# Optimization experiments

Hardware: AMD Instinct MI355X
Metric: run time of the kernel (lower is better)

## Reference

```python
import jax, jax.numpy as jnp
import numpy as np

N = 100000
E = 3200000
D = 64


def setup_inputs() -> dict:
    key = jax.random.key(0)
    k1, k2, k3 = jax.random.split(key, 3)
    indices = jax.random.randint(k1, (2, E), 0, N, dtype=jnp.int64) if jax.config.jax_enable_x64 else jax.random.randint(k1, (2, E), 0, N, dtype=jnp.int32)
    values = jax.random.uniform(k2, (E,), dtype=jnp.float32)
    b = jax.random.normal(k3, (N, D), dtype=jnp.float32)
    return {"indices": indices, "values": values, "shape": N, "b": b}


def reference(indices, values, shape, b):
    # sparse COO [N,N] @ dense [N,D]:
    # out[r] = sum over edges e with row[e]==r of values[e] * b[col[e]]
    row, col = indices[0], indices[1]
    msgs = values[:, None] * b[col]            # [E, D] gather + scale
    out = jax.ops.segment_sum(msgs, row, num_segments=shape)  # [N, D] scatter-add
    return out
```

## Files before the change

### kernel.cpp

```cpp
#include <hip/hip_runtime.h>
#include <hip/hip_bf16.h>


#define D 64
#define BROWS 64
#define MAXNB 2048
#define CAP 2560
#define NM (CAP / 256)
#define SPILLCAP 8192
#define NCHUNK 4
#define NBINS (BROWS * NCHUNK)

#define CROWS 2048
#define NCB 64
#define NREP 8
#define SCH_A 4096
#define CBLK 4352
#define NBLK_C 16
#define CAPC8 (CBLK * 2)
#define NCONV 1024

__global__ __launch_bounds__(256) void spmm_atomic_kernel(
    const int* __restrict__ rows, const int* __restrict__ cols,
    const float* __restrict__ vals, const float* __restrict__ b,
    float* __restrict__ out, int E) {
  long long gid = (long long)blockIdx.x * blockDim.x + threadIdx.x;
  int e = (int)(gid >> 6);
  int d = (int)(gid & 63);
  if (e >= E) return;
  atomicAdd(&out[(long long)rows[e] * D + d], vals[e] * b[(long long)cols[e] * D + d]);
}

__device__ __forceinline__ unsigned bf16rne(float x) {
  unsigned u = __float_as_uint(x);
  return (u + 0x7FFFu + ((u >> 16) & 1u)) >> 16;
}
__global__ __launch_bounds__(256) void coarse_conv_kernel(
    const int* __restrict__ rows, const int* __restrict__ cols,
    const float* __restrict__ vals, int* __restrict__ gcoarse,
    uint2* __restrict__ cslab_lo, uint2* __restrict__ cslab_hi, int csplitV,
    uint4* __restrict__ spill, int* __restrict__ spill_cnt, int E, int nco,
    const float4* __restrict__ bsrc, uint2* __restrict__ b16, int n4) {
  __shared__ uint2 stage[SCH_A];
  __shared__ unsigned char sbin[SCH_A];
  __shared__ int h[NCB];
  __shared__ int lst[NCB];
  __shared__ int gb[NCB];
  int t = threadIdx.x;

  if (blockIdx.x >= nco) {
    for (int i = (blockIdx.x - nco) * 256 + t; i < n4; i += NCONV * 256) {
      float4 f = bsrc[i];
      b16[i] = make_uint2(bf16rne(f.x) | (bf16rne(f.y) << 16),
                          bf16rne(f.z) | (bf16rne(f.w) << 16));
    }
    return;
  }

  int rep = blockIdx.x & (NREP - 1);
  if (t < NCB) h[t] = 0;
  __syncthreads();
  int start = blockIdx.x * SCH_A;
  int ec = E - start;
  if (ec > SCH_A) ec = SCH_A;
  bool full = (start + SCH_A <= E);

  int4 r4[4];
  int rank[16];
  if (full) {
#pragma unroll
    for (int ki = 0; ki < 4; ki++) {
      r4[ki] = ((const int4*)(rows + start + ki * 1024))[t];
      rank[4 * ki + 0] = atomicAdd(&h[r4[ki].x >> 11], 1);
      rank[4 * ki + 1] = atomicAdd(&h[r4[ki].y >> 11], 1);
      rank[4 * ki + 2] = atomicAdd(&h[r4[ki].z >> 11], 1);
      rank[4 * ki + 3] = atomicAdd(&h[r4[ki].w >> 11], 1);
    }
  } else {
#pragma unroll
    for (int ki = 0; ki < 4; ki++) {
      int e = start + ki * 1024 + t * 4;
      int4 rr = make_int4(-1, -1, -1, -1);
      if (e + 0 < E) { rr.x = rows[e + 0]; rank[4 * ki + 0] = atomicAdd(&h[rr.x >> 11], 1); }
      if (e + 1 < E) { rr.y = rows[e + 1]; rank[4 * ki + 1] = atomicAdd(&h[rr.y >> 11], 1); }
      if (e + 2 < E) { rr.z = rows[e + 2]; rank[4 * ki + 2] = atomicAdd(&h[rr.z >> 11], 1); }
      if (e + 3 < E) { rr.w = rows[e + 3]; rank[4 * ki + 3] = atomicAdd(&h[rr.w >> 11], 1); }
      r4[ki] = rr;
    }
  }
  __syncthreads();
  if (t < NCB) {
    int c = h[t];
    int x = c;
#pragma unroll
    for (int off = 1; off < 64; off <<= 1) {
      int u = __shfl_up(x, off);
      if (t >= off) x += u;
    }
    lst[t] = x - c;
    gb[t] = c ? atomicAdd(&gcoarse[t * NREP + rep], c) : 0;
  }
  __syncthreads();
#pragma unroll
  for (int ki = 0; ki < 4; ki++) {
    int e = start + ki * 1024 + t * 4;
    int rr[4] = {r4[ki].x, r4[ki].y, r4[ki].z, r4[ki].w};
    int cc[4];
    float vv[4];
    if (full) {
      int4 c4 = ((const int4*)(cols + start + ki * 1024))[t];
      float4 v4 = ((const float4*)(vals + start + ki * 1024))[t];
      cc[0] = c4.x; cc[1] = c4.y; cc[2] = c4.z; cc[3] = c4.w;
      vv[0] = v4.x; vv[1] = v4.y; vv[2] = v4.z; vv[3] = v4.w;
    } else {
#pragma unroll
      for (int j = 0; j < 4; j++) {
        cc[j] = (e + j < E) ? cols[e + j] : 0;
        vv[j] = (e + j < E) ? vals[e + j] : 0.f;
      }
    }
#pragma unroll
    for (int j = 0; j < 4; j++) {
      if (e + j < E) {
        int r = rr[j];
        int bn = r >> 11;
        int pos = lst[bn] + rank[4 * ki + j];
        stage[pos] = make_uint2(((unsigned)(r & (CROWS - 1)) << 17) |
                                    (unsigned)cc[j],
                                __float_as_uint(vv[j]));
        sbin[pos] = (unsigned char)bn;
      }
    }
  }
  __syncthreads();
  for (int i = t; i < ec; i += 256) {
    int bn = sbin[i];
    uint2 p = stage[i];
    int pin = gb[bn] + (i - lst[bn]);
    if (pin < CAPC8) {
      int v = bn * NREP + rep;
      uint2* slab = (v < csplitV) ? (cslab_lo + (size_t)v * CAPC8)
                                  : (cslab_hi + (size_t)(v - csplitV) * CAPC8);
      slab[pin] = p;
    } else {
      int sp = atomicAdd(spill_cnt, 1);
      if (sp < SPILLCAP)
        spill[sp] = make_uint4((unsigned)((bn << 11) | (int)(p.x >> 17)),
                               p.x & 0x1FFFFu, p.y, 0u);
    }
  }
}

__global__ __launch_bounds__(256) void fine_scatter_kernel(
    const int* __restrict__ gcoarse, const uint2* __restrict__ cslab_lo,
    const uint2* __restrict__ cslab_hi, int csplitV, int* __restrict__ gcount,
    uint2* __restrict__ pairs, uint4* __restrict__ spill,
    int* __restrict__ spill_cnt) {
  int c = blockIdx.x >> 4;
  int sub = blockIdx.x & 15;
  int v = c * NREP + (sub >> 1);
  int cnt = gcoarse[v];
  if (cnt > CAPC8) cnt = CAPC8;
  int base = (sub & 1) * CBLK;
  int ec = cnt - base;
  if (ec <= 0) return;
  if (ec > CBLK) ec = CBLK;
  const uint2* src = ((v < csplitV) ? (cslab_lo + (size_t)v * CAPC8)
                                    : (cslab_hi + (size_t)(v - csplitV) * CAPC8)) +
                     base;
  __shared__ uint2 stage[CBLK];
  __shared__ unsigned char sbin[CBLK];
  __shared__ int h[32];
  __shared__ int lst[32];
  __shared__ int gb[32];
  int t = threadIdx.x;
  if (t < 32) h[t] = 0;
  __syncthreads();
  uint2 mine[17];
  int rank[17];
#pragma unroll
  for (int k = 0; k < 17; k++) {
    int i = k * 256 + t;
    if (i < ec) {
      mine[k] = src[i];
      rank[k] = atomicAdd(&h[mine[k].x >> 23], 1);
    }
  }
  __syncthreads();
  if (t < 32) {
    int cn = h[t];
    int x = cn;
#pragma unroll
    for (int off = 1; off < 32; off <<= 1) {
      int u = __shfl_up(x, off);
      if (t >= off) x += u;
    }
    lst[t] = x - cn;
    gb[t] = cn ? atomicAdd(&gcount[c * 32 + t], cn) : 0;
  }
  __syncthreads();
#pragma unroll
  for (int k = 0; k < 17; k++) {
    int i = k * 256 + t;
    if (i < ec) {
      uint2 p = mine[k];
      int f = (int)(p.x >> 23);
      int pos = lst[f] + rank[k];
      unsigned key2 = (((p.x >> 17) & 63u) << 26) | ((p.x & 0x1FFFFu) << 7);
      stage[pos] = make_uint2(key2, p.y);
      sbin[pos] = (unsigned char)f;
    }
  }
  __syncthreads();
  for (int i = t; i < ec; i += 256) {
    int f = sbin[i];
    uint2 p = stage[i];
    int pin = gb[f] + (i - lst[f]);
    int gbkt = c * 32 + f;
    if (pin < CAP) {
      pairs[(size_t)gbkt * CAP + pin] = p;
    } else {
      int sp = atomicAdd(spill_cnt, 1);
      if (sp < SPILLCAP)
        spill[sp] = make_uint4((unsigned)(gbkt * BROWS + (int)(p.x >> 26)),
                               (p.x >> 7) & 0x1FFFFu, p.y, 0u);
    }
  }
}

__global__ __launch_bounds__(256) void spmm_fused_kernel(
    const uint2* __restrict__ pairs, const int* __restrict__ gcount,
    const uint2* __restrict__ b16, float* __restrict__ out, int N,
    const uint4* __restrict__ spill, const int* __restrict__ spill_cnt) {
  __shared__ uint2 lp[CAP];
  __shared__ int cnt[NBINS];
  __shared__ int roff[NBINS + 1];
  __shared__ int wpart[4];
  int bkt = blockIdx.x;
  int cntE = gcount[bkt];
  if (cntE > CAP) cntE = CAP;
  const uint2* src = pairs + (size_t)bkt * CAP;
  int t = threadIdx.x;
  int lane = t & 63;
  int wv = t >> 6;
  if (t < NBINS) cnt[t] = 0;
  __syncthreads();
  uint2 mine[NM];
  int rk[NM];
#pragma unroll
  for (int k = 0; k < NM; k++) {
    int i = t + k * 256;
    if (i < cntE) {
      mine[k] = src[i];
      int bin = ((mine[k].x >> 26) << 2) | ((mine[k].x >> 22) & 3);
      rk[k] = atomicAdd(&cnt[bin], 1);
    }
  }
  __syncthreads();
  {
    int c0 = cnt[t];
    int x = c0;
#pragma unroll
    for (int off = 1; off < 64; off <<= 1) {
      int u = __shfl_up(x, off);
      if (lane >= off) x += u;
    }
    if (lane == 63) wpart[wv] = x;
    __syncthreads();
    int wbase = 0;
    for (int w = 0; w < wv; w++) wbase += wpart[w];
    roff[t] = wbase + x - c0;
    if (t == 255) roff[NBINS] = wbase + x;
  }
  __syncthreads();
#pragma unroll
  for (int k = 0; k < NM; k++) {
    int i = t + k * 256;
    if (i < cntE) {
      int bin = ((mine[k].x >> 26) << 2) | ((mine[k].x >> 22) & 3);
      lp[roff[bin] + rk[k]] = make_uint2(mine[k].x & 0x03FFFF80u, mine[k].y);
    }
  }
  __syncthreads();
  int g = lane >> 3;
  int l8 = lane & 7;
  int gid32 = wv * 8 + g;
  const char* bq = (const char*)b16 + (l8 << 4);
  int row_base = bkt * BROWS;
  float acc[2][8] = {{0.f, 0.f, 0.f, 0.f, 0.f, 0.f, 0.f, 0.f},
                     {0.f, 0.f, 0.f, 0.f, 0.f, 0.f, 0.f, 0.f}};
  for (int ch = 0; ch < NCHUNK; ch++) {
#pragma unroll
    for (int rr = 0; rr < 2; rr++) {
      int r = gid32 + 32 * rr;
      int bin = (r << 2) | ch;
      int j0 = roff[bin], j1 = roff[bin + 1];
      for (int base = j0; base < j1; base += 4) {
        uint4 bv[4];
        float vv[4];
#pragma unroll
        for (int k = 0; k < 4; k++) {
          int idx = base + k;
          int ic = (idx < j1) ? idx : j0;
          uint2 p = lp[ic];
          bv[k] = *(const uint4*)(bq + p.x);
          vv[k] = (idx < j1) ? __uint_as_float(p.y) : 0.f;
        }
#pragma unroll
        for (int k = 0; k < 4; k++) {
          unsigned u0 = bv[k].x, u1 = bv[k].y, u2 = bv[k].z, u3 = bv[k].w;
          float v = vv[k];
          acc[rr][0] += v * __uint_as_float(u0 << 16);
          acc[rr][1] += v * __uint_as_float(u0 & 0xFFFF0000u);
          acc[rr][2] += v * __uint_as_float(u1 << 16);
          acc[rr][3] += v * __uint_as_float(u1 & 0xFFFF0000u);
          acc[rr][4] += v * __uint_as_float(u2 << 16);
          acc[rr][5] += v * __uint_as_float(u2 & 0xFFFF0000u);
          acc[rr][6] += v * __uint_as_float(u3 << 16);
          acc[rr][7] += v * __uint_as_float(u3 & 0xFFFF0000u);
        }
      }
    }
  }
  int nsp = *spill_cnt;
  if (nsp > 0) {
    if (nsp > SPILLCAP) nsp = SPILLCAP;
    for (int s = 0; s < nsp; s++) {
      uint4 e = spill[s];
      int rg = (int)e.x;
      if ((rg >> 6) != bkt) continue;
      int rl = rg & 63;
#pragma unroll
      for (int rr = 0; rr < 2; rr++) {
        if (rl == gid32 + 32 * rr) {
          uint4 bv = *(const uint4*)((const char*)b16 +
                                     ((size_t)e.y << 7) + (l8 << 4));
          float v = __uint_as_float(e.z);
          acc[rr][0] += v * __uint_as_float(bv.x << 16);
          acc[rr][1] += v * __uint_as_float(bv.x & 0xFFFF0000u);
          acc[rr][2] += v * __uint_as_float(bv.y << 16);
          acc[rr][3] += v * __uint_as_float(bv.y & 0xFFFF0000u);
          acc[rr][4] += v * __uint_as_float(bv.z << 16);
          acc[rr][5] += v * __uint_as_float(bv.z & 0xFFFF0000u);
          acc[rr][6] += v * __uint_as_float(bv.w << 16);
          acc[rr][7] += v * __uint_as_float(bv.w & 0xFFFF0000u);
        }
      }
    }
  }
#pragma unroll
  for (int rr = 0; rr < 2; rr++) {
    int gr = row_base + gid32 + 32 * rr;
    if (gr < N) {
      float4* dst = (float4*)(out + (size_t)gr * D + l8 * 8);
      dst[0] = make_float4(acc[rr][0], acc[rr][1], acc[rr][2], acc[rr][3]);
      dst[1] = make_float4(acc[rr][4], acc[rr][5], acc[rr][6], acc[rr][7]);
    }
  }
}

extern "C" void kernel_launch(void* const* d_in, const int* in_sizes, int n_in,
                              void* d_out, int out_size, void* d_ws, size_t ws_size,
                              hipStream_t stream) {
  const int* indices = (const int*)d_in[0];
  const float* vals  = (const float*)d_in[1];
  const float* b     = (const float*)d_in[3];

  int E = in_sizes[1];
  int N = in_sizes[3] / D;
  const int* rows = indices;
  const int* cols = indices + E;

  int NC = (N + CROWS - 1) / CROWS;
  int NCV = NC * NREP;
  int n4 = N * D / 4;

  size_t off_gcount  = 0;
  size_t off_gcoarse = off_gcount + (size_t)MAXNB * 4;
  size_t off_scnt    = off_gcoarse + (size_t)NCB * NREP * 4;
  size_t off_spill   = (off_scnt + 4 + 15) & ~(size_t)15;
  size_t off_pairs   = off_spill + (size_t)SPILLCAP * 16;
  size_t npbkt       = (size_t)NC * 32;
  size_t off_b16     = off_pairs + npbkt * CAP * 8;
  size_t off_cextra  = off_b16 + (size_t)N * D * 2;
  size_t outbytes    = (size_t)out_size * 4;
  int csplitV = (int)(outbytes / ((size_t)CAPC8 * 8));
  if (csplitV > NCV) csplitV = NCV;
  size_t cextra = (size_t)(NCV - csplitV) * CAPC8 * 8;
  size_t need2 = off_cextra + cextra;

  if (ws_size >= need2 && NC <= NCB && (int)npbkt <= MAXNB) {
    char*  ws        = (char*)d_ws;
    int*   gcount    = (int*)(ws + off_gcount);
    int*   gcoarse   = (int*)(ws + off_gcoarse);
    int*   spill_cnt = (int*)(ws + off_scnt);
    uint4* spill     = (uint4*)(ws + off_spill);
    uint2* pairs     = (uint2*)(ws + off_pairs);
    uint2* b16       = (uint2*)(ws + off_b16);
    uint2* cslab_lo  = (uint2*)d_out;
    uint2* cslab_hi  = (uint2*)(ws + off_cextra);

    hipMemsetAsync(gcount, 0,
                   (size_t)MAXNB * 4 + (size_t)NCB * NREP * 4 + 4, stream);
    int nco = (E + SCH_A - 1) / SCH_A;
    coarse_conv_kernel<<<nco + NCONV, 256, 0, stream>>>(
        rows, cols, vals, gcoarse, cslab_lo, cslab_hi, csplitV,
        spill, spill_cnt, E, nco, (const float4*)b, b16, n4);
    fine_scatter_kernel<<<NC * NBLK_C, 256, 0, stream>>>(
        gcoarse, cslab_lo, cslab_hi, csplitV, gcount, pairs, spill, spill_cnt);
    spmm_fused_kernel<<<(int)npbkt, 256, 0, stream>>>(
        pairs, gcount, b16, (float*)d_out, N, spill, spill_cnt);
    return;
  }

  hipMemsetAsync(d_out, 0, (size_t)out_size * sizeof(float), stream);
  long long total = (long long)E * 64;
  spmm_atomic_kernel<<<(int)((total + 255) / 256), 256, 0, stream>>>(
      rows, cols, vals, b, (float*)d_out, E);
}
```

Baseline: 212.3 us.

## Drop fine scatter pass; fused kernel filters coarse slabs directly per bucket

Removes the fine_scatter kernel and its pairs buffer. Each fused SpMM block now scans all 8 replica slabs of its coarse row group twice, once to count and once to place, keeping only entries for its 64-row bucket. A shared-memory overflow list and a block-index swizzle for L2 locality are added. This removes one kernel launch and a global write/read of all edges, but each block now reads 32x more slab data than it keeps (filtering), which relies on L2 reuse across sibling buckets.

```diff
diff --git a/kernel.cpp b/kernel.cpp
--- a/kernel.cpp
+++ b/kernel.cpp
@@ -4,20 +4,17 @@
 
 #define D 64
 #define BROWS 64
-#define MAXNB 2048
 #define CAP 2560
-#define NM (CAP / 256)
 #define SPILLCAP 8192
 #define NCHUNK 4
 #define NBINS (BROWS * NCHUNK)
+#define OVFCAP 64
 
 #define CROWS 2048
 #define NCB 64
 #define NREP 8
 #define SCH_A 4096
-#define CBLK 4352
-#define NBLK_C 16
-#define CAPC8 (CBLK * 2)
+#define CAPC8 8704
 #define NCONV 1024
 
 __global__ __launch_bounds__(256) void spmm_atomic_kernel(
@@ -38,7 +35,7 @@
 __global__ __launch_bounds__(256) void coarse_conv_kernel(
     const int* __restrict__ rows, const int* __restrict__ cols,
     const float* __restrict__ vals, int* __restrict__ gcoarse,
-    uint2* __restrict__ cslab_lo, uint2* __restrict__ cslab_hi, int csplitV,
+    uint2* __restrict__ cslab,
     uint4* __restrict__ spill, int* __restrict__ spill_cnt, int E, int nco,
     const float4* __restrict__ bsrc, uint2* __restrict__ b16, int n4) {
   __shared__ uint2 stage[SCH_A];
@@ -138,10 +135,7 @@
     uint2 p = stage[i];
     int pin = gb[bn] + (i - lst[bn]);
     if (pin < CAPC8) {
-      int v = bn * NREP + rep;
-      uint2* slab = (v < csplitV) ? (cslab_lo + (size_t)v * CAPC8)
-                                  : (cslab_hi + (size_t)(v - csplitV) * CAPC8);
-      slab[pin] = p;
+      cslab[(size_t)(bn * NREP + rep) * CAPC8 + pin] = p;
     } else {
       int sp = atomicAdd(spill_cnt, 1);
       if (sp < SPILLCAP)
@@ -151,109 +145,36 @@
   }
 }
 
-__global__ __launch_bounds__(256) void fine_scatter_kernel(
-    const int* __restrict__ gcoarse, const uint2* __restrict__ cslab_lo,
-    const uint2* __restrict__ cslab_hi, int csplitV, int* __restrict__ gcount,
-    uint2* __restrict__ pairs, uint4* __restrict__ spill,
-    int* __restrict__ spill_cnt) {
-  int c = blockIdx.x >> 4;
-  int sub = blockIdx.x & 15;
-  int v = c * NREP + (sub >> 1);
-  int cnt = gcoarse[v];
-  if (cnt > CAPC8) cnt = CAPC8;
-  int base = (sub & 1) * CBLK;
-  int ec = cnt - base;
-  if (ec <= 0) return;
-  if (ec > CBLK) ec = CBLK;
-  const uint2* src = ((v < csplitV) ? (cslab_lo + (size_t)v * CAPC8)
-                                    : (cslab_hi + (size_t)(v - csplitV) * CAPC8)) +
-                     base;
-  __shared__ uint2 stage[CBLK];
-  __shared__ unsigned char sbin[CBLK];
-  __shared__ int h[32];
-  __shared__ int lst[32];
-  __shared__ int gb[32];
-  int t = threadIdx.x;
-  if (t < 32) h[t] = 0;
-  __syncthreads();
-  uint2 mine[17];
-  int rank[17];
-#pragma unroll
-  for (int k = 0; k < 17; k++) {
-    int i = k * 256 + t;
-    if (i < ec) {
-      mine[k] = src[i];
-      rank[k] = atomicAdd(&h[mine[k].x >> 23], 1);
-    }
-  }
-  __syncthreads();
-  if (t < 32) {
-    int cn = h[t];
-    int x = cn;
-#pragma unroll
-    for (int off = 1; off < 32; off <<= 1) {
-      int u = __shfl_up(x, off);
-      if (t >= off) x += u;
-    }
-    lst[t] = x - cn;
-    gb[t] = cn ? atomicAdd(&gcount[c * 32 + t], cn) : 0;
-  }
-  __syncthreads();
-#pragma unroll
-  for (int k = 0; k < 17; k++) {
-    int i = k * 256 + t;
-    if (i < ec) {
-      uint2 p = mine[k];
-      int f = (int)(p.x >> 23);
-      int pos = lst[f] + rank[k];
-      unsigned key2 = (((p.x >> 17) & 63u) << 26) | ((p.x & 0x1FFFFu) << 7);
-      stage[pos] = make_uint2(key2, p.y);
-      sbin[pos] = (unsigned char)f;
-    }
-  }
-  __syncthreads();
-  for (int i = t; i < ec; i += 256) {
-    int f = sbin[i];
-    uint2 p = stage[i];
-    int pin = gb[f] + (i - lst[f]);
-    int gbkt = c * 32 + f;
-    if (pin < CAP) {
-      pairs[(size_t)gbkt * CAP + pin] = p;
-    } else {
-      int sp = atomicAdd(spill_cnt, 1);
-      if (sp < SPILLCAP)
-        spill[sp] = make_uint4((unsigned)(gbkt * BROWS + (int)(p.x >> 26)),
-                               (p.x >> 7) & 0x1FFFFu, p.y, 0u);
-    }
-  }
-}
-
 __global__ __launch_bounds__(256) void spmm_fused_kernel(
-    const uint2* __restrict__ pairs, const int* __restrict__ gcount,
-    const uint2* __restrict__ b16, float* __restrict__ out, int N,
+    const int* __restrict__ gcoarse, const uint2* __restrict__ cslab,
+    const uint2* __restrict__ b16, float* __restrict__ out, int N, int swz,
     const uint4* __restrict__ spill, const int* __restrict__ spill_cnt) {
   __shared__ uint2 lp[CAP];
   __shared__ int cnt[NBINS];
   __shared__ int roff[NBINS + 1];
+  __shared__ int wcur[NBINS];
   __shared__ int wpart[4];
-  int bkt = blockIdx.x;
-  int cntE = gcount[bkt];
-  if (cntE > CAP) cntE = CAP;
-  const uint2* src = pairs + (size_t)bkt * CAP;
+  __shared__ uint2 ovf[OVFCAP];
+  __shared__ int ovfn;
+  int bid = blockIdx.x;
+  int bkt = swz ? ((bid & 7) * swz + (bid >> 3)) : bid;
+  int c = bkt >> 5;
+  unsigned f = (unsigned)(bkt & 31);
   int t = threadIdx.x;
   int lane = t & 63;
   int wv = t >> 6;
   if (t < NBINS) cnt[t] = 0;
-  __syncthreads();
-  uint2 mine[NM];
-  int rk[NM];
-#pragma unroll
-  for (int k = 0; k < NM; k++) {
-    int i = t + k * 256;
-    if (i < cntE) {
-      mine[k] = src[i];
-      int bin = ((mine[k].x >> 26) << 2) | ((mine[k].x >> 22) & 3);
-      rk[k] = atomicAdd(&cnt[bin], 1);
+  if (t == 0) ovfn = 0;
+  __syncthreads();
+  for (int rep = 0; rep < NREP; rep++) {
+    int v = c * NREP + rep;
+    int cr = gcoarse[v];
+    if (cr > CAPC8) cr = CAPC8;
+    const uint2* src = cslab + (size_t)v * CAPC8;
+    for (int i = t; i < cr; i += 256) {
+      unsigned k = src[i].x;
+      if (((k >> 23) & 31u) == f)
+        atomicAdd(&cnt[((int)((k >> 17) & 63u) << 2) | (int)((k >> 15) & 3u)], 1);
     }
   }
   __syncthreads();
@@ -270,15 +191,30 @@
     int wbase = 0;
     for (int w = 0; w < wv; w++) wbase += wpart[w];
     roff[t] = wbase + x - c0;
+    wcur[t] = wbase + x - c0;
     if (t == 255) roff[NBINS] = wbase + x;
   }
   __syncthreads();
-#pragma unroll
-  for (int k = 0; k < NM; k++) {
-    int i = t + k * 256;
-    if (i < cntE) {
-      int bin = ((mine[k].x >> 26) << 2) | ((mine[k].x >> 22) & 3);
-      lp[roff[bin] + rk[k]] = make_uint2(mine[k].x & 0x03FFFF80u, mine[k].y);
+  for (int rep = 0; rep < NREP; rep++) {
+    int v = c * NREP + rep;
+    int cr = gcoarse[v];
+    if (cr > CAPC8) cr = CAPC8;
+    const uint2* src = cslab + (size_t)v * CAPC8;
+    for (int i = t; i < cr; i += 256) {
+      uint2 p = src[i];
+      if (((p.x >> 23) & 31u) == f) {
+        int bin = ((int)((p.x >> 17) & 63u) << 2) | (int)((p.x >> 15) & 3u);
+        int pos = atomicAdd(&wcur[bin], 1);
+        if (pos < CAP) {
+          lp[pos] = make_uint2((p.x & 0x1FFFFu) << 7, p.y);
+        } else {
+          int o = atomicAdd(&ovfn, 1);
+          if (o < OVFCAP)
+            ovf[o] = make_uint2(((p.x >> 17) & 63u) << 26 |
+                                    ((p.x & 0x1FFFFu) << 7),
+                                p.y);
+        }
+      }
     }
   }
   __syncthreads();
@@ -295,6 +231,8 @@
       int r = gid32 + 32 * rr;
       int bin = (r << 2) | ch;
       int j0 = roff[bin], j1 = roff[bin + 1];
+      if (j0 > CAP) j0 = CAP;
+      if (j1 > CAP) j1 = CAP;
       for (int base = j0; base < j1; base += 4) {
         uint4 bv[4];
         float vv[4];
@@ -319,6 +257,28 @@
           acc[rr][6] += v * __uint_as_float(u3 << 16);
           acc[rr][7] += v * __uint_as_float(u3 & 0xFFFF0000u);
         }
+      }
+    }
+  }
+  int nov = ovfn;
+  if (nov > OVFCAP) nov = OVFCAP;
+  for (int s = 0; s < nov; s++) {
+    uint2 e = ovf[s];
+    int rl = (int)(e.x >> 26);
+    unsigned boff = e.x & 0x03FFFF80u;
+#pragma unroll
+    for (int rr = 0; rr < 2; rr++) {
+      if (rl == gid32 + 32 * rr) {
+        uint4 bv = *(const uint4*)((const char*)b16 + boff + (l8 << 4));
+        float v = __uint_as_float(e.y);
+        acc[rr][0] += v * __uint_as_float(bv.x << 16);
+        acc[rr][1] += v * __uint_as_float(bv.x & 0xFFFF0000u);
+        acc[rr][2] += v * __uint_as_float(bv.y << 16);
+        acc[rr][3] += v * __uint_as_float(bv.y & 0xFFFF0000u);
+        acc[rr][4] += v * __uint_as_float(bv.z << 16);
+        acc[rr][5] += v * __uint_as_float(bv.z & 0xFFFF0000u);
+        acc[rr][6] += v * __uint_as_float(bv.w << 16);
+        acc[rr][7] += v * __uint_as_float(bv.w & 0xFFFF0000u);
       }
     }
   }
@@ -373,43 +333,32 @@
 
   int NC = (N + CROWS - 1) / CROWS;
   int NCV = NC * NREP;
+  int npbkt = NC * 32;
   int n4 = N * D / 4;
 
-  size_t off_gcount  = 0;
-  size_t off_gcoarse = off_gcount + (size_t)MAXNB * 4;
-  size_t off_scnt    = off_gcoarse + (size_t)NCB * NREP * 4;
+  size_t off_gcoarse = 0;
+  size_t off_scnt    = (size_t)NCB * NREP * 4;
   size_t off_spill   = (off_scnt + 4 + 15) & ~(size_t)15;
-  size_t off_pairs   = off_spill + (size_t)SPILLCAP * 16;
-  size_t npbkt       = (size_t)NC * 32;
-  size_t off_b16     = off_pairs + npbkt * CAP * 8;
-  size_t off_cextra  = off_b16 + (size_t)N * D * 2;
-  size_t outbytes    = (size_t)out_size * 4;
-  int csplitV = (int)(outbytes / ((size_t)CAPC8 * 8));
-  if (csplitV > NCV) csplitV = NCV;
-  size_t cextra = (size_t)(NCV - csplitV) * CAPC8 * 8;
-  size_t need2 = off_cextra + cextra;
-
-  if (ws_size >= need2 && NC <= NCB && (int)npbkt <= MAXNB) {
+  size_t off_b16     = off_spill + (size_t)SPILLCAP * 16;
+  size_t off_cslab   = off_b16 + (size_t)N * D * 2;
+  size_t need        = off_cslab + (size_t)NCV * CAPC8 * 8;
+
+  if (ws_size >= need && NC <= NCB) {
     char*  ws        = (char*)d_ws;
-    int*   gcount    = (int*)(ws + off_gcount);
     int*   gcoarse   = (int*)(ws + off_gcoarse);
     int*   spill_cnt = (int*)(ws + off_scnt);
     uint4* spill     = (uint4*)(ws + off_spill);
-    uint2* pairs     = (uint2*)(ws + off_pairs);
     uint2* b16       = (uint2*)(ws + off_b16);
-    uint2* cslab_lo  = (uint2*)d_out;
-    uint2* cslab_hi  = (uint2*)(ws + off_cextra);
-
-    hipMemsetAsync(gcount, 0,
-                   (size_t)MAXNB * 4 + (size_t)NCB * NREP * 4 + 4, stream);
+    uint2* cslab     = (uint2*)(ws + off_cslab);
+
+    hipMemsetAsync(gcoarse, 0, (size_t)NCB * NREP * 4 + 4, stream);
     int nco = (E + SCH_A - 1) / SCH_A;
     coarse_conv_kernel<<<nco + NCONV, 256, 0, stream>>>(
-        rows, cols, vals, gcoarse, cslab_lo, cslab_hi, csplitV,
-        spill, spill_cnt, E, nco, (const float4*)b, b16, n4);
-    fine_scatter_kernel<<<NC * NBLK_C, 256, 0, stream>>>(
-        gcoarse, cslab_lo, cslab_hi, csplitV, gcount, pairs, spill, spill_cnt);
-    spmm_fused_kernel<<<(int)npbkt, 256, 0, stream>>>(
-        pairs, gcount, b16, (float*)d_out, N, spill, spill_cnt);
+        rows, cols, vals, gcoarse, cslab, spill, spill_cnt, E, nco,
+        (const float4*)b, b16, n4);
+    int swz = (npbkt % 8 == 0) ? npbkt / 8 : 0;
+    spmm_fused_kernel<<<npbkt, 256, 0, stream>>>(
+        gcoarse, cslab, b16, (float*)d_out, N, swz, spill, spill_cnt);
     return;
   }
 
```

Measured after the change: 474.8 us. 2.24x slower.
